# Kernel tuning notes

Measured on AMD Instinct MI355X. Metric: run time of the kernel, lower is better.

Reference implementation:

```python
import jax, jax.numpy as jnp
import numpy as np
from jax import lax

R = 3
D = (2 * R + 1) ** 2  # 49 local offsets


def _unfold(x, r):
    # torch F.unfold(kernel=2r+1, padding=r): (B,C,H,W) -> (B, C*K*K, H, W),
    # channel-major (c, ky, kx) ordering, matching conv_general_dilated_patches.
    k = 2 * r + 1
    return lax.conv_general_dilated_patches(
        x, (k, k), (1, 1), [(r, r), (r, r)],
        dimension_numbers=("NCHW", "OIHW", "NCHW"))


def _l2norm(x, eps=1e-12):
    n = jnp.sqrt(jnp.sum(x * x, axis=1, keepdims=True))
    return x / jnp.maximum(n, eps)


def setup_inputs() -> dict:
    key = jax.random.key(0)
    ks = jax.random.split(key, 8)
    B, Cin, Cmid, H, W = 2, 256, 128, 112, 112
    phi_cur = jax.random.normal(ks[0], (B, Cin, H, W), jnp.float32)
    phi_rnd = jax.random.normal(ks[1], (B, Cin, H, W), jnp.float32)
    P_cur = jax.random.normal(ks[2], (B, 3, H, W), jnp.float32)
    P_rnd = jax.random.normal(ks[3], (B, 3, H, W), jnp.float32)
    Wq = jax.random.normal(ks[4], (Cmid, Cin), jnp.float32) * 0.05
    Wk = jax.random.normal(ks[5], (Cmid, Cin), jnp.float32) * 0.05
    Wv = jax.random.normal(ks[6], (D, D), jnp.float32) * 0.1
    bv = jnp.zeros((D,), jnp.float32)
    gamma = jnp.array(1.0, jnp.float32)
    return dict(phi_cur=phi_cur, phi_rnd=phi_rnd, P_cur=P_cur, P_rnd=P_rnd,
                Wq=Wq, Wk=Wk, Wv=Wv, bv=bv, gamma=gamma)


def reference(phi_cur, phi_rnd, P_cur, P_rnd, Wq, Wk, Wv, bv, gamma):
    B, _, H, W = phi_cur.shape
    # 1x1 convs + channel L2 normalize
    q = _l2norm(jnp.einsum('oc,bchw->bohw', Wq, phi_cur))
    k = _l2norm(jnp.einsum('oc,bchw->bohw', Wk, phi_rnd))
    # local cost volume: patches (B, Cmid, D, H, W)
    patches = _unfold(k, R).reshape(B, -1, D, H, W)
    corr = jnp.einsum('bchw,bcdhw->bdhw', q, patches)  # (B,D,H,W)
    vol_corr = jnp.einsum('ed,bdhw->behw', Wv, corr) + bv[None, :, None, None]
    # geometric bias
    Pr = _unfold(P_rnd, R).reshape(B, 3, D, H, W)
    dP = P_cur[:, :, None, :, :] - Pr  # (B,3,D,H,W)
    dz = dP[:, 2]
    dist = jnp.sqrt(jnp.clip(jnp.sum(dP * dP, axis=1), 1e-12, None))
    logits = vol_corr + gamma * (-dist - 0.5 * jnp.abs(dz))
    w = jax.nn.softmax(logits, axis=1)
    off = jnp.arange(-R, R + 1, dtype=w.dtype)
    dY, dX = jnp.meshgrid(off, off, indexing='ij')
    offx = dX.reshape(1, D, 1, 1)
    offy = dY.reshape(1, D, 1, 1)
    du = jnp.sum(w * offx, axis=1, keepdims=True)
    dv = jnp.sum(w * offy, axis=1, keepdims=True)
    conf = jnp.max(w, axis=1, keepdims=True)
    return du, dv, conf
```

## Files before the change

### kernel.cpp

```cpp
#include <hip/hip_runtime.h>
#include <hip/hip_bf16.h>
#include <math.h>

constexpr int B    = 2;
constexpr int CIN  = 256;
constexpr int CMID = 128;
constexpr int H    = 112;
constexpr int W    = 112;
constexpr int HW   = H * W;
constexpr int NPIX = B * HW;
constexpr int RAD  = 3;
constexpr int KS   = 7;
constexpr int DD   = 49;

typedef __attribute__((ext_vector_type(8))) short  short8;
typedef __attribute__((ext_vector_type(4))) float  float4v;

__device__ __forceinline__ unsigned pkbf(float a, float b) {
    union { __hip_bfloat162 h; unsigned u; } c;
    c.h = __float22bfloat162_rn(make_float2(a, b));
    return c.u;
}

__global__ __launch_bounds__(256) void build_wv2(
    const float* __restrict__ Wvm, float2* __restrict__ wv2)
{
    const int j = blockIdx.x * 256 + threadIdx.x;
    if (j < 25 * DD) {
        const int e2 = j / DD, d = j % DD;
        const float a  = Wvm[d * DD + 2 * e2];
        const float bb = (2 * e2 + 1 < DD) ? Wvm[d * DD + 2 * e2 + 1] : 0.f;
        wv2[j] = make_float2(a, bb);
    }
}

constexpr int PSTR = 264;

__global__ __launch_bounds__(256) void proj_mfma(
    const float* __restrict__ phi_cur, const float* __restrict__ phi_rnd,
    const float* __restrict__ Wq, const float* __restrict__ Wk,
    unsigned short* __restrict__ q_ws, unsigned short* __restrict__ k_ws)
{
    __shared__ unsigned short pt[64 * PSTR];
    __shared__ float red[4][64];

    const int tid  = threadIdx.x;
    const int lane = tid & 63;
    const int wv   = __builtin_amdgcn_readfirstlane(tid >> 6);
    const int t    = blockIdx.y;

    const float* __restrict__ phi = t ? phi_rnd : phi_cur;
    const float* __restrict__ Wm  = t ? Wk : Wq;
    unsigned short* __restrict__ outp = t ? k_ws : q_ws;

    const int pgb = blockIdx.x * 64;
    const int b   = pgb / HW;
    const int pim = pgb % HW;
    const float* pbase = phi + (size_t)b * CIN * HW + pim;

#pragma unroll
    for (int pass = 0; pass < 8; ++pass) {
        const int idx = pass * 256 + tid;
        const int cp  = idx >> 4;
        const int pq  = idx & 15;
        const int c0  = cp * 2;
        const float4 va = *(const float4*)(pbase + (size_t)c0 * HW + pq * 4);
        const float4 vb = *(const float4*)(pbase + (size_t)(c0 + 1) * HW + pq * 4);
        *(unsigned*)(pt + (pq * 4 + 0) * PSTR + c0) = pkbf(va.x, vb.x);
        *(unsigned*)(pt + (pq * 4 + 1) * PSTR + c0) = pkbf(va.y, vb.y);
        *(unsigned*)(pt + (pq * 4 + 2) * PSTR + c0) = pkbf(va.z, vb.z);
        *(unsigned*)(pt + (pq * 4 + 3) * PSTR + c0) = pkbf(va.w, vb.w);
    }

    const int m = lane & 15, quad = lane >> 4;
    short8 af[2][8];
#pragma unroll
    for (int ot = 0; ot < 2; ++ot)
#pragma unroll
        for (int kc = 0; kc < 8; ++kc) {
            const float* wr = Wm + (size_t)(wv * 32 + ot * 16 + m) * CIN
                                 + kc * 32 + quad * 8;
            const float4 w0 = *(const float4*)(wr);
            const float4 w1 = *(const float4*)(wr + 4);
            union { short8 s; unsigned u[4]; } pk;
            pk.u[0] = pkbf(w0.x, w0.y);
            pk.u[1] = pkbf(w0.z, w0.w);
            pk.u[2] = pkbf(w1.x, w1.y);
            pk.u[3] = pkbf(w1.z, w1.w);
            af[ot][kc] = pk.s;
        }

    __syncthreads();

    float4v acc[2][4];
#pragma unroll
    for (int ot = 0; ot < 2; ++ot)
#pragma unroll
        for (int nt = 0; nt < 4; ++nt) acc[ot][nt] = (float4v)0.f;

#pragma unroll
    for (int kc = 0; kc < 8; ++kc) {
        short8 bf[4];
#pragma unroll
        for (int nt = 0; nt < 4; ++nt)
            bf[nt] = *(const short8*)(pt + (nt * 16 + m) * PSTR + kc * 32 + quad * 8);
#pragma unroll
        for (int ot = 0; ot < 2; ++ot)
#pragma unroll
            for (int nt = 0; nt < 4; ++nt)
                acc[ot][nt] = __builtin_amdgcn_mfma_f32_16x16x32_bf16(
                    af[ot][kc], bf[nt], acc[ot][nt], 0, 0, 0);
    }

#pragma unroll
    for (int nt = 0; nt < 4; ++nt) {
        float ss = 0.f;
#pragma unroll
        for (int ot = 0; ot < 2; ++ot)
#pragma unroll
            for (int r = 0; r < 4; ++r)
                ss = fmaf(acc[ot][nt][r], acc[ot][nt][r], ss);
        ss += __shfl_xor(ss, 16, 64);
        ss += __shfl_xor(ss, 32, 64);
        if (quad == 0) red[wv][nt * 16 + m] = ss;
    }
    __syncthreads();

    float inv[4];
#pragma unroll
    for (int nt = 0; nt < 4; ++nt) {
        const int px = nt * 16 + m;
        const float tot = red[0][px] + red[1][px] + red[2][px] + red[3][px];
        inv[nt] = 1.f / fmaxf(sqrtf(tot), 1e-12f);
    }

#pragma unroll
    for (int nt = 0; nt < 4; ++nt)
#pragma unroll
        for (int ot = 0; ot < 2; ++ot) {
            uint2 st;
            st.x = pkbf(acc[ot][nt][0] * inv[nt], acc[ot][nt][1] * inv[nt]);
            st.y = pkbf(acc[ot][nt][2] * inv[nt], acc[ot][nt][3] * inv[nt]);
            *(uint2*)(outp + (size_t)(pgb + nt * 16 + m) * CMID
                      + wv * 32 + ot * 16 + quad * 4) = st;
        }
}

constexpr int TILE = 16;
constexpr int COLS = TILE + 6;
constexpr int NV   = KS * COLS;
constexpr int KSTR = 136;

__global__ __launch_bounds__(256, 3) void corr_kernel(
    const unsigned short* __restrict__ q_ws, const unsigned short* __restrict__ k_ws,
    const float* __restrict__ P_cur, const float* __restrict__ P_rnd,
    const float2* __restrict__ wv2, const float* __restrict__ bv,
    const float* __restrict__ gamma_p, float* __restrict__ out)
{
    __shared__ unsigned short kt[NV * KSTR];
    __shared__ unsigned short qt[TILE * KSTR];
    __shared__ float cs[TILE][52];
    __shared__ float prt[3 * NV];

    const int tid  = threadIdx.x;
    const int lane = tid & 63;
    const int wv   = __builtin_amdgcn_readfirstlane(tid >> 6);
    const int w0   = blockIdx.x * TILE;
    const int h    = blockIdx.y;
    const int b    = blockIdx.z;

    const int sub  = tid & 15;
    const int vgrp = tid >> 4;
#pragma unroll
    for (int pass = 0; pass < 10; ++pass) {
        const int vi = pass * 16 + vgrp;
        if (vi < NV) {
            const int rr = vi / COLS;
            const int cc = vi % COLS;
            const int hh = h + rr - RAD;
            const int ww = w0 + cc - RAD;
            uint4 v = make_uint4(0, 0, 0, 0);
            if (hh >= 0 && hh < H && ww >= 0 && ww < W)
                v = *(const uint4*)(k_ws + (size_t)(b * HW + hh * W + ww) * CMID + sub * 8);
            *(uint4*)(kt + vi * KSTR + sub * 8) = v;
        }
    }
    {
        const uint4 v = *(const uint4*)(q_ws + (size_t)(b * HW + h * W + w0 + vgrp) * CMID + sub * 8);
        *(uint4*)(qt + vgrp * KSTR + sub * 8) = v;
    }
#pragma unroll
    for (int pass = 0; pass < 2; ++pass) {
        const int idx = pass * 256 + tid;
        if (idx < 3 * NV) {
            const int ch = idx / NV;
            const int vi = idx % NV;
            const int rr = vi / COLS;
            const int cc = vi % COLS;
            const int hh = h + rr - RAD;
            const int ww = w0 + cc - RAD;
            float v = 0.f;
            if (hh >= 0 && hh < H && ww >= 0 && ww < W)
                v = P_rnd[((size_t)b * 3 + ch) * HW + hh * W + ww];
            prt[idx] = v;
        }
    }

    const int  ld    = (lane < DD) ? lane : 0;
    const bool valid = (lane < DD);
    float wrow[52];
#pragma unroll
    for (int e2 = 0; e2 < 25; ++e2) {
        const float2 v = wv2[e2 * DD + ld];
        wrow[2 * e2]     = v.x;
        wrow[2 * e2 + 1] = v.y;
    }
    wrow[50] = wrow[51] = 0.f;
    const float bvv   = bv[ld];
    const float gamma = gamma_p[0];

    __syncthreads();

    if (tid < TILE * 3)
        cs[tid / 3][49 + tid % 3] = 0.f;

    const int m = lane & 15, quad = lane >> 4;
    for (int g = wv; g < 14; g += 4) {
        const int r  = g >> 1;
        const int nt = g & 1;
        const int vi = min(r * COLS + nt * 16 + m, NV - 1);
        float4v acc = (float4v)0.f;
#pragma unroll
        for (int kc = 0; kc < 4; ++kc) {
            const short8 afrag = *(const short8*)(qt + m * KSTR + kc * 32 + quad * 8);
            const short8 bfrag = *(const short8*)(kt + vi * KSTR + kc * 32 + quad * 8);
            acc = __builtin_amdgcn_mfma_f32_16x16x32_bf16(afrag, bfrag, acc, 0, 0, 0);
        }
#pragma unroll
        for (int reg = 0; reg < 4; ++reg) {
            const int p   = quad * 4 + reg;
            const int off = nt * 16 + m - p;
            if (off >= 0 && off <= 6)
                cs[p][r * 7 + off] = acc[reg];
        }
    }
    __syncthreads();

    const int dyr = ld / KS;
    const int dxc = ld % KS;
    const int dy  = dyr - RAD;
    const int dx  = dxc - RAD;
    const float fdx = (float)dx, fdy = (float)dy;

    for (int i = 0; i < 4; ++i) {
        const int pl = wv * 4 + i;
        const int pg = b * HW + h * W + w0 + pl;

        const int vi = dyr * COLS + pl + dxc;
        const float rx = prt[vi];
        const float ry = prt[NV + vi];
        const float rz = prt[2 * NV + vi];
        const float* pc = P_cur + (size_t)b * 3 * HW + (h * W + w0 + pl);
        const float cx = pc[0], cy = pc[HW], cz = pc[2 * HW];
        const float dpx = cx - rx, dpy = cy - ry, dpz = cz - rz;
        const float dist = sqrtf(fmaxf(dpx * dpx + dpy * dpy + dpz * dpz, 1e-12f));

        float logit = -INFINITY;
        if (valid) {
            float v = bvv;
#pragma unroll
            for (int e4 = 0; e4 < 13; ++e4) {
                const float4 c4 = *(const float4*)&cs[pl][e4 * 4];
                v = fmaf(wrow[e4 * 4 + 0], c4.x, v);
                v = fmaf(wrow[e4 * 4 + 1], c4.y, v);
                v = fmaf(wrow[e4 * 4 + 2], c4.z, v);
                v = fmaf(wrow[e4 * 4 + 3], c4.w, v);
            }
            logit = v + gamma * (-dist - 0.5f * fabsf(dpz));
        }

        float lmax = logit;
#pragma unroll
        for (int off = 32; off; off >>= 1)
            lmax = fmaxf(lmax, __shfl_xor(lmax, off, 64));
        const float e1 = valid ? __expf(logit - lmax) : 0.f;

        float s0 = e1, s1 = e1 * fdx, s2 = e1 * fdy;
#pragma unroll
        for (int off = 32; off; off >>= 1) {
            s0 += __shfl_xor(s0, off, 64);
            s1 += __shfl_xor(s1, off, 64);
            s2 += __shfl_xor(s2, off, 64);
        }

        if (lane == 0) {
            const float rZ = 1.f / s0;
            out[pg]            = s1 * rZ;
            out[NPIX + pg]     = s2 * rZ;
            out[2 * NPIX + pg] = rZ;
        }
    }
}

extern "C" void kernel_launch(void* const* d_in, const int* in_sizes, int n_in,
                              void* d_out, int out_size, void* d_ws, size_t ws_size,
                              hipStream_t stream)
{
    const float* phi_cur = (const float*)d_in[0];
    const float* phi_rnd = (const float*)d_in[1];
    const float* P_cur   = (const float*)d_in[2];
    const float* P_rnd   = (const float*)d_in[3];
    const float* Wq      = (const float*)d_in[4];
    const float* Wk      = (const float*)d_in[5];
    const float* Wv      = (const float*)d_in[6];
    const float* bv      = (const float*)d_in[7];
    const float* gm      = (const float*)d_in[8];
    float* out = (float*)d_out;

    unsigned short* ws   = (unsigned short*)d_ws;
    unsigned short* q_ws = ws;
    unsigned short* k_ws = q_ws + (size_t)NPIX * CMID;
    float2* wv2 = (float2*)(k_ws + (size_t)NPIX * CMID);

    build_wv2<<<dim3((25 * DD + 255) / 256), 256, 0, stream>>>(Wv, wv2);

    proj_mfma<<<dim3(NPIX / 64, 2), 256, 0, stream>>>(
        phi_cur, phi_rnd, Wq, Wk, q_ws, k_ws);

    corr_kernel<<<dim3(W / TILE, H, B), 256, 0, stream>>>(
        q_ws, k_ws, P_cur, P_rnd, wv2, bv, gm, out);
}
```

Baseline: 150.2 us.

## Load MFMA fragments directly from global, drop LDS staging and Wv prep kernel

The correlation kernel no longer stages the k halo tile and q tile in shared memory. It reads bf16 MFMA fragments straight from global memory and zero-fills out-of-bounds neighbours. The separate build_wv2 launch is removed, and each lane now loads its Wv row directly. The occupancy hint rises from 3 to 4 blocks per CU, and the first barrier is dropped. This removes LDS traffic, one barrier and one kernel launch, at the cost of strided, uncoalesced Wv loads and reliance on the caches for neighbour reuse.

```diff
diff --git a/kernel.cpp b/kernel.cpp
--- a/kernel.cpp
+++ b/kernel.cpp
@@ -20,18 +20,6 @@
     union { __hip_bfloat162 h; unsigned u; } c;
     c.h = __float22bfloat162_rn(make_float2(a, b));
     return c.u;
-}
-
-__global__ __launch_bounds__(256) void build_wv2(
-    const float* __restrict__ Wvm, float2* __restrict__ wv2)
-{
-    const int j = blockIdx.x * 256 + threadIdx.x;
-    if (j < 25 * DD) {
-        const int e2 = j / DD, d = j % DD;
-        const float a  = Wvm[d * DD + 2 * e2];
-        const float bb = (2 * e2 + 1 < DD) ? Wvm[d * DD + 2 * e2 + 1] : 0.f;
-        wv2[j] = make_float2(a, bb);
-    }
 }
 
 constexpr int PSTR = 264;
@@ -149,16 +137,13 @@
 constexpr int TILE = 16;
 constexpr int COLS = TILE + 6;
 constexpr int NV   = KS * COLS;
-constexpr int KSTR = 136;
-
-__global__ __launch_bounds__(256, 3) void corr_kernel(
+
+__global__ __launch_bounds__(256, 4) void corr_kernel(
     const unsigned short* __restrict__ q_ws, const unsigned short* __restrict__ k_ws,
     const float* __restrict__ P_cur, const float* __restrict__ P_rnd,
-    const float2* __restrict__ wv2, const float* __restrict__ bv,
+    const float* __restrict__ Wvm, const float* __restrict__ bv,
     const float* __restrict__ gamma_p, float* __restrict__ out)
 {
-    __shared__ unsigned short kt[NV * KSTR];
-    __shared__ unsigned short qt[TILE * KSTR];
     __shared__ float cs[TILE][52];
     __shared__ float prt[3 * NV];
 
@@ -169,26 +154,6 @@
     const int h    = blockIdx.y;
     const int b    = blockIdx.z;
 
-    const int sub  = tid & 15;
-    const int vgrp = tid >> 4;
-#pragma unroll
-    for (int pass = 0; pass < 10; ++pass) {
-        const int vi = pass * 16 + vgrp;
-        if (vi < NV) {
-            const int rr = vi / COLS;
-            const int cc = vi % COLS;
-            const int hh = h + rr - RAD;
-            const int ww = w0 + cc - RAD;
-            uint4 v = make_uint4(0, 0, 0, 0);
-            if (hh >= 0 && hh < H && ww >= 0 && ww < W)
-                v = *(const uint4*)(k_ws + (size_t)(b * HW + hh * W + ww) * CMID + sub * 8);
-            *(uint4*)(kt + vi * KSTR + sub * 8) = v;
-        }
-    }
-    {
-        const uint4 v = *(const uint4*)(q_ws + (size_t)(b * HW + h * W + w0 + vgrp) * CMID + sub * 8);
-        *(uint4*)(qt + vgrp * KSTR + sub * 8) = v;
-    }
 #pragma unroll
     for (int pass = 0; pass < 2; ++pass) {
         const int idx = pass * 256 + tid;
@@ -206,34 +171,37 @@
         }
     }
 
+    if (tid < TILE * 3)
+        cs[tid / 3][49 + tid % 3] = 0.f;
+
     const int  ld    = (lane < DD) ? lane : 0;
     const bool valid = (lane < DD);
     float wrow[52];
 #pragma unroll
-    for (int e2 = 0; e2 < 25; ++e2) {
-        const float2 v = wv2[e2 * DD + ld];
-        wrow[2 * e2]     = v.x;
-        wrow[2 * e2 + 1] = v.y;
-    }
-    wrow[50] = wrow[51] = 0.f;
+    for (int e = 0; e < DD; ++e) wrow[e] = Wvm[ld * DD + e];
+    wrow[49] = wrow[50] = wrow[51] = 0.f;
     const float bvv   = bv[ld];
     const float gamma = gamma_p[0];
 
-    __syncthreads();
-
-    if (tid < TILE * 3)
-        cs[tid / 3][49 + tid % 3] = 0.f;
-
     const int m = lane & 15, quad = lane >> 4;
+    const unsigned short* qbase =
+        q_ws + (size_t)(b * HW + h * W + w0 + m) * CMID + quad * 8;
+
     for (int g = wv; g < 14; g += 4) {
         const int r  = g >> 1;
         const int nt = g & 1;
-        const int vi = min(r * COLS + nt * 16 + m, NV - 1);
+        const int hh = h + r - RAD;
+        const int ww = w0 + nt * 16 + m - RAD;
+        const bool inb = (hh >= 0) && (hh < H) && (ww >= 0) && (ww < W);
+        const unsigned short* kbase =
+            k_ws + (size_t)(b * HW + hh * W + ww) * CMID + quad * 8;
+
         float4v acc = (float4v)0.f;
 #pragma unroll
         for (int kc = 0; kc < 4; ++kc) {
-            const short8 afrag = *(const short8*)(qt + m * KSTR + kc * 32 + quad * 8);
-            const short8 bfrag = *(const short8*)(kt + vi * KSTR + kc * 32 + quad * 8);
+            const short8 afrag = *(const short8*)(qbase + kc * 32);
+            const short8 bfrag = inb ? *(const short8*)(kbase + kc * 32)
+                                     : (short8)0;
             acc = __builtin_amdgcn_mfma_f32_16x16x32_bf16(afrag, bfrag, acc, 0, 0, 0);
         }
 #pragma unroll
@@ -320,13 +288,10 @@
     unsigned short* ws   = (unsigned short*)d_ws;
     unsigned short* q_ws = ws;
     unsigned short* k_ws = q_ws + (size_t)NPIX * CMID;
-    float2* wv2 = (float2*)(k_ws + (size_t)NPIX * CMID);
-
-    build_wv2<<<dim3((25 * DD + 255) / 256), 256, 0, stream>>>(Wv, wv2);
 
     proj_mfma<<<dim3(NPIX / 64, 2), 256, 0, stream>>>(
         phi_cur, phi_rnd, Wq, Wk, q_ws, k_ws);
 
     corr_kernel<<<dim3(W / TILE, H, B), 256, 0, stream>>>(
-        q_ws, k_ws, P_cur, P_rnd, wv2, bv, gm, out);
-}
+        q_ws, k_ws, P_cur, P_rnd, Wv, bv, gm, out);
+}
```

Measured after the change: 148.0 us. About the same (-1.5%).
